# Kernel tuning notes

Measured on AMD Instinct MI355X. Metric: run time of the kernel, lower is better.

## Reference

```python
import jax, jax.numpy as jnp
import numpy as np

B, L, IN = 16, 1024, 128
H, C = 4, 32


def setup_inputs() -> dict:
    key = jax.random.key(0)
    k1, k2, k3, k4, k5, k6 = jax.random.split(key, 6)
    x = jax.random.normal(k1, (B, L, IN), dtype=jnp.float32)
    adj = jax.random.randint(k2, (B, L, L), 0, 2, dtype=jnp.int32)
    # xavier-uniform-ish scales
    s_w = (6.0 / (IN + H * C)) ** 0.5
    W = jax.random.uniform(k3, (H * C, IN), jnp.float32, -s_w, s_w)
    b = jnp.zeros((H * C,), jnp.float32)
    s_a = (6.0 / (1 + C)) ** 0.5
    att_src = jax.random.uniform(k4, (1, H, C), jnp.float32, -s_a, s_a)
    att_dst = jax.random.uniform(k5, (1, H, C), jnp.float32, -s_a, s_a)
    return {"x": x, "adj": adj, "W": W, "b": b, "att_src": att_src, "att_dst": att_dst}


def reference(x, adj, W, b, att_src, att_dst):
    Bx, Lx, _ = x.shape
    Hh, Cc = att_src.shape[1], att_src.shape[2]
    # dropout p=0.0 -> identity
    xp = (x @ W.T + b).reshape(Bx, Lx, Hh, Cc)            # (B,L,H,C)
    a_src = jnp.einsum('blhc,hc->bhl', xp, att_src[0])    # (B,H,L)
    a_dst = jnp.einsum('blhc,hc->bhl', xp, att_dst[0])    # (B,H,L)
    # scores[b,h,i,j] = leaky_relu(a_src[j] + a_dst[i])
    scores = jax.nn.leaky_relu(a_src[:, :, None, :] + a_dst[:, :, :, None], negative_slope=0.2)
    eye = jnp.eye(Lx, dtype=bool)
    mask = jnp.where((adj > 0) | eye, 0.0, -jnp.inf)      # (B,L,L)
    alpha = jax.nn.softmax(scores + mask[:, None, :, :], axis=-1)  # (B,H,L,L)
    out = jnp.einsum('bhij,bjhc->bihc', alpha, xp)        # (B,L,H,C)
    return out.reshape(Bx, Lx, Hh * Cc)
```

## Files before the change

### kernel.cpp

```cpp
#include <hip/hip_runtime.h>
#include <hip/hip_bf16.h>

typedef __bf16 bf16x8 __attribute__((ext_vector_type(8)));
typedef _Float16 f16x8 __attribute__((ext_vector_type(8)));
typedef _Float16 f16x2 __attribute__((ext_vector_type(2)));
typedef float f32x4 __attribute__((ext_vector_type(4)));

#define B_DIM 16
#define L_DIM 1024
#define H_DIM 4
#define HC 128
#define TI 64
#define WPITCH 136

__global__ __launch_bounds__(256) void mask_pack_kernel(
    const int* __restrict__ adj, unsigned* __restrict__ mask_g)
{
  const int t = threadIdx.x;
  const int wv = t >> 6, lane = t & 63;
  const int row0 = blockIdx.x * 8 + wv * 2;
  const int* base = adj + (size_t)row0 * L_DIM;

  int4 av[8];
#pragma unroll
  for (int c = 0; c < 4; ++c) {
    av[c]     = *reinterpret_cast<const int4*>(base + c * 256 + lane * 4);
    av[c + 4] = *reinterpret_cast<const int4*>(base + 1024 + c * 256 + lane * 4);
  }

#pragma unroll
  for (int r = 0; r < 2; ++r) {
    const int row = row0 + r;
    const int i = row & (L_DIM - 1);
#pragma unroll
    for (int c = 0; c < 4; ++c) {
      const int4 u = av[r * 4 + c];
      unsigned b4 = (unsigned)u.x | ((unsigned)u.y << 1) |
                    ((unsigned)u.z << 2) | ((unsigned)u.w << 3);
      unsigned p;
      p = __shfl_xor(b4, 1);
      unsigned b8  = (lane & 1) ? (p | (b4 << 4))   : (b4 | (p << 4));
      p = __shfl_xor(b8, 2);
      unsigned b16 = (lane & 2) ? (p | (b8 << 8))   : (b8 | (p << 8));
      p = __shfl_xor(b16, 4);
      unsigned b32 = (lane & 4) ? (p | (b16 << 16)) : (b16 | (p << 16));
      const int widx = c * 8 + (lane >> 3);
      if ((i >> 5) == widx) b32 |= (1u << (i & 31));
      if ((lane & 7) == 0) mask_g[(size_t)row * 32 + widx] = b32;
    }
  }
}

__global__ __launch_bounds__(128) void proj_kernel(
    const float* __restrict__ x, const float* __restrict__ W,
    const float* __restrict__ bias, const float* __restrict__ att_src,
    const float* __restrict__ att_dst, _Float16* __restrict__ xpT,
    _Float16* __restrict__ E1h, _Float16* __restrict__ E2h,
    float* __restrict__ Rr)
{
  __shared__ __align__(16) __bf16 Wlds[128 * WPITCH];
  __shared__ __align__(16) __bf16 xh[32 * WPITCH];
  __shared__ __align__(16) __bf16 xl[32 * WPITCH];
  const int t = threadIdx.x;
  const int w = t >> 6;
  const int lane = t & 63;
  const int r0 = blockIdx.x * 32;

#pragma unroll
  for (int p = 0; p < 16; ++p) {
    const int idx = p * 1024 + t * 8;
    const int n = idx >> 7, k = idx & 127;
    const f32x4 a = *reinterpret_cast<const f32x4*>(W + idx);
    const f32x4 b = *reinterpret_cast<const f32x4*>(W + idx + 4);
    bf16x8 v;
#pragma unroll
    for (int e = 0; e < 4; ++e) { v[e] = (__bf16)a[e]; v[e + 4] = (__bf16)b[e]; }
    *reinterpret_cast<bf16x8*>(&Wlds[n * WPITCH + k]) = v;
  }
#pragma unroll
  for (int p = 0; p < 4; ++p) {
    const int idx = p * 1024 + t * 8;
    const int r = idx >> 7, k = idx & 127;
    const float* xp_ = x + (size_t)(r0 + r) * 128 + k;
    const f32x4 a = *reinterpret_cast<const f32x4*>(xp_);
    const f32x4 b = *reinterpret_cast<const f32x4*>(xp_ + 4);
    bf16x8 vh, vl;
#pragma unroll
    for (int e = 0; e < 4; ++e) {
      const float fa = a[e], fb = b[e];
      vh[e] = (__bf16)fa;          vh[e + 4] = (__bf16)fb;
      vl[e] = (__bf16)(fa - (float)vh[e]);
      vl[e + 4] = (__bf16)(fb - (float)vh[e + 4]);
    }
    *reinterpret_cast<bf16x8*>(&xh[r * WPITCH + k]) = vh;
    *reinterpret_cast<bf16x8*>(&xl[r * WPITCH + k]) = vl;
  }
  __syncthreads();

  const int rr = lane & 15;
  const int g8 = (lane >> 4) * 8;
  f32x4 acc[8] = {};
#pragma unroll
  for (int kk = 0; kk < 4; ++kk) {
    const int ko = kk * 32 + g8;
    const bf16x8 bh = *reinterpret_cast<const bf16x8*>(&xh[(w * 16 + rr) * WPITCH + ko]);
    const bf16x8 bl = *reinterpret_cast<const bf16x8*>(&xl[(w * 16 + rr) * WPITCH + ko]);
#pragma unroll
    for (int nc = 0; nc < 8; ++nc) {
      const bf16x8 af = *reinterpret_cast<const bf16x8*>(&Wlds[(nc * 16 + rr) * WPITCH + ko]);
      acc[nc] = __builtin_amdgcn_mfma_f32_16x16x32_bf16(af, bh, acc[nc], 0, 0, 0);
      acc[nc] = __builtin_amdgcn_mfma_f32_16x16x32_bf16(af, bl, acc[nc], 0, 0, 0);
    }
  }

  const int q4 = (lane >> 4) * 4;
  const int grow = r0 + w * 16 + rr;
  const int bb = grow >> 10;
  const int lg = grow & 1023;
  float asum[4] = {0.f, 0.f, 0.f, 0.f};
  float adsum[4] = {0.f, 0.f, 0.f, 0.f};
#pragma unroll
  for (int nc = 0; nc < 8; ++nc) {
    const int n0 = nc * 16 + q4;
    const f32x4 bv = *reinterpret_cast<const f32x4*>(bias + n0);
    const f32x4 sv = *reinterpret_cast<const f32x4*>(att_src + n0);
    const f32x4 dv = *reinterpret_cast<const f32x4*>(att_dst + n0);
    const int h = nc >> 1;
#pragma unroll
    for (int reg = 0; reg < 4; ++reg) {
      const float v = acc[nc][reg] + bv[reg];
      const int n = n0 + reg;
      xpT[((size_t)bb * 128 + n) * 1024 + lg] = (_Float16)v;
      asum[h]  = fmaf(v, sv[reg], asum[h]);
      adsum[h] = fmaf(v, dv[reg], adsum[h]);
    }
  }
#pragma unroll
  for (int h = 0; h < 4; ++h) {
    asum[h]  += __shfl_xor(asum[h], 16);
    asum[h]  += __shfl_xor(asum[h], 32);
    adsum[h] += __shfl_xor(adsum[h], 16);
    adsum[h] += __shfl_xor(adsum[h], 32);
  }
  if ((lane >> 4) == 0) {
#pragma unroll
    for (int h = 0; h < 4; ++h) {
      const size_t o = ((size_t)bb * 4 + h) * 1024 + lg;
      E1h[o] = (_Float16)(16.0f * __expf(asum[h]));
      E2h[o] = (_Float16)__expf(0.2f * asum[h]);
      Rr[o]  = 16.0f * __expf(-0.8f * adsum[h]);
    }
  }
}

__global__ __launch_bounds__(512, 4) void gat_attn_kernel(
    const unsigned* __restrict__ mask_g, const _Float16* __restrict__ xpT,
    const _Float16* __restrict__ E1h, const _Float16* __restrict__ E2h,
    const float* __restrict__ Rr, float* __restrict__ out)
{
  __shared__ __align__(16) char smem[53248];
  unsigned* e1u = reinterpret_cast<unsigned*>(smem);
  unsigned* e2u = reinterpret_cast<unsigned*>(smem + 8192);
  unsigned char* msk = reinterpret_cast<unsigned char*>(smem + 16384);
  float* comb = reinterpret_cast<float*>(smem);

  const int wg  = blockIdx.x;
  const int xcd = wg & 7;
  const int idx = wg >> 3;
  const int b   = xcd * 2 + (idx & 1);
  const int i0  = (idx >> 1) * TI;

  const int t = threadIdx.x;
  const int wv = t >> 6;
  const int lane = t & 63;
  const int h  = wv >> 1;
  const int jh = wv & 1;

  {
    const int r = t >> 3, sg = t & 7;
    const uint4 m = *reinterpret_cast<const uint4*>(
        mask_g + ((size_t)b * L_DIM + i0 + r) * 32 + sg * 4);
    *reinterpret_cast<uint4*>(&msk[r * 176 + sg * 16]) = m;
  }
  {
    const int sh = t >> 7;
    const int off = (t & 127) * 8;
    const _Float16* p1 = E1h + ((size_t)(b * H_DIM + sh)) * L_DIM + off;
    const _Float16* p2 = E2h + ((size_t)(b * H_DIM + sh)) * L_DIM + off;
    *reinterpret_cast<uint4*>(&e1u[sh * 512 + (off >> 1)]) = *reinterpret_cast<const uint4*>(p1);
    *reinterpret_cast<uint4*>(&e2u[sh * 512 + (off >> 1)]) = *reinterpret_cast<const uint4*>(p2);
  }
  __syncthreads();

  const int ln15 = lane & 15;
  const int kh = lane >> 4;
  const int jb = kh * 8;
  const int base = jh * 512;
  const float* RrB = Rr + ((size_t)(b * H_DIM + h)) * L_DIM + i0 + ln15;
  f16x2 R2g[4];
#pragma unroll
  for (int g = 0; g < 4; ++g) {
    const _Float16 rh = (_Float16)RrB[g * 16];
    R2g[g][0] = rh; R2g[g][1] = rh;
  }
  const _Float16* xb0 = xpT + ((size_t)(b * 128 + h * 32 + ln15)) * 1024 + base;
  const _Float16* xb1 = xb0 + 16 * 1024;

  f32x4 acc0[4] = {}, acc1[4] = {}, accS[4] = {};
  f16x8 ones16;
#pragma unroll
  for (int e = 0; e < 8; ++e) ones16[e] = (_Float16)1.0f;

  uint4 pf0[2], pf1[2];
#pragma unroll
  for (int s = 0; s < 2; ++s) {
    pf0[s] = *reinterpret_cast<const uint4*>(xb0 + s * 32 + jb);
    pf1[s] = *reinterpret_cast<const uint4*>(xb1 + s * 32 + jb);
  }
  uint4 u1c = *reinterpret_cast<const uint4*>(&e1u[h * 512 + ((base + jb) >> 1)]);
  uint4 u2c = *reinterpret_cast<const uint4*>(&e2u[h * 512 + ((base + jb) >> 1)]);

#pragma unroll 4
  for (int kr = 0; kr < 512; kr += 32) {
    const int k0 = base + kr;
    const int wb = jh * 64 + ((kr >> 5) << 2);
    unsigned mb[4];
#pragma unroll
    for (int g = 0; g < 4; ++g) {
      const unsigned w32 = *reinterpret_cast<const unsigned*>(
          &msk[(g * 16 + ln15) * 176 + wb]);
      mb[g] = (w32 >> (kh * 8)) & 0xffu;
    }

    const int kn = (((k0 + 32) & 1023) + jb) >> 1;
    const uint4 u1n = *reinterpret_cast<const uint4*>(&e1u[h * 512 + kn]);
    const uint4 u2n = *reinterpret_cast<const uint4*>(&e2u[h * 512 + kn]);

    const int sl = (kr >> 5) & 1;
    const uint4 bb0 = pf0[sl];
    const uint4 bb1 = pf1[sl];
    pf0[sl] = *reinterpret_cast<const uint4*>(xb0 + kr + 64 + jb);
    pf1[sl] = *reinterpret_cast<const uint4*>(xb1 + kr + 64 + jb);

    const unsigned uu1[4] = {u1c.x, u1c.y, u1c.z, u1c.w};
    const unsigned uu2[4] = {u2c.x, u2c.y, u2c.z, u2c.w};
    unsigned rg[4][4];
#pragma unroll
    for (int q = 0; q < 4; ++q) {
      f16x2 a, ee;
      __builtin_memcpy(&a,  &uu1[q], 4);
      __builtin_memcpy(&ee, &uu2[q], 4);
#pragma unroll
      for (int g = 0; g < 4; ++g) {
        const f16x2 pr = ee * R2g[g];
        const f16x2 mx = __builtin_elementwise_max(a, pr);
        unsigned mu;
        __builtin_memcpy(&mu, &mx, 4);
        const unsigned mlo = (mb[g] & (1u << (2 * q)))     ? 0xFFFFu : 0u;
        const unsigned mhi = (mb[g] & (1u << (2 * q + 1))) ? 0xFFFF0000u : 0u;
        rg[g][q] = mu & (mlo | mhi);
      }
    }
    f16x8 b0h, b1h;
    __builtin_memcpy(&b0h, &bb0, 16);
    __builtin_memcpy(&b1h, &bb1, 16);
#pragma unroll
    for (int g = 0; g < 4; ++g) {
      const uint4 afu = {rg[g][0], rg[g][1], rg[g][2], rg[g][3]};
      f16x8 af;
      __builtin_memcpy(&af, &afu, 16);
      acc0[g] = __builtin_amdgcn_mfma_f32_16x16x32_f16(af, b0h, acc0[g], 0, 0, 0);
      acc1[g] = __builtin_amdgcn_mfma_f32_16x16x32_f16(af, b1h, acc1[g], 0, 0, 0);
      accS[g] = __builtin_amdgcn_mfma_f32_16x16x32_f16(af, ones16, accS[g], 0, 0, 0);
    }
    u1c = u1n; u2c = u2n;
  }

  __syncthreads();
  if (jh == 1) {
#pragma unroll
    for (int g = 0; g < 4; ++g) {
      float* cp = &comb[((h * 4 + g) * 64 + lane) * 13];
#pragma unroll
      for (int e = 0; e < 4; ++e) {
        cp[e]     = acc0[g][e];
        cp[4 + e] = acc1[g][e];
        cp[8 + e] = accS[g][e];
      }
    }
  }
  __syncthreads();
  if (jh == 0) {
#pragma unroll
    for (int g = 0; g < 4; ++g) {
      const float* cp = &comb[((h * 4 + g) * 64 + lane) * 13];
#pragma unroll
      for (int reg = 0; reg < 4; ++reg) {
        const float s = accS[g][reg] + cp[8 + reg];
        const float rs = 1.0f / s;
        float* op = out + ((size_t)(b * L_DIM + i0 + g * 16 + kh * 4 + reg)) * HC + h * 32;
        op[ln15]      = (acc0[g][reg] + cp[reg])     * rs;
        op[16 + ln15] = (acc1[g][reg] + cp[4 + reg]) * rs;
      }
    }
  }
}

extern "C" void kernel_launch(void* const* d_in, const int* in_sizes, int n_in,
                              void* d_out, int out_size, void* d_ws, size_t ws_size,
                              hipStream_t stream) {
  (void)in_sizes; (void)n_in; (void)out_size; (void)ws_size;
  const float* x        = (const float*)d_in[0];
  const int*   adj      = (const int*)d_in[1];
  const float* W        = (const float*)d_in[2];
  const float* bias     = (const float*)d_in[3];
  const float* att_src  = (const float*)d_in[4];
  const float* att_dst  = (const float*)d_in[5];
  float* out = (float*)d_out;

  char* ws = (char*)d_ws;
  _Float16* xpT    = (_Float16*)ws;
  _Float16* E1h    = (_Float16*)(ws + (size_t)4 * 1024 * 1024);
  _Float16* E2h    = (_Float16*)(ws + (size_t)4 * 1024 * 1024 + 131072);
  float*    Rr     = (float*)(ws + (size_t)4 * 1024 * 1024 + 262144);
  unsigned* mask_g = (unsigned*)(ws + (size_t)4 * 1024 * 1024 + 524288);

  hipLaunchKernelGGL(mask_pack_kernel, dim3(B_DIM * L_DIM / 8), dim3(256), 0, stream,
                     adj, mask_g);
  hipLaunchKernelGGL(proj_kernel, dim3(B_DIM * L_DIM / 32), dim3(128), 0, stream,
                     x, W, bias, att_src, att_dst, xpT, E1h, E2h, Rr);
  hipLaunchKernelGGL(gat_attn_kernel, dim3(B_DIM * L_DIM / TI), dim3(512), 0, stream,
                     mask_g, xpT, E1h, E2h, Rr, out);
}
```

Measured before the change: 41.33 us.

## Merge mask-pack and projection kernels; split attention key range across four waves

```diff
diff --git a/kernel.cpp b/kernel.cpp
--- a/kernel.cpp
+++ b/kernel.cpp
@@ -12,63 +12,60 @@
 #define HC 128
 #define TI 64
 #define WPITCH 136
-
-__global__ __launch_bounds__(256) void mask_pack_kernel(
-    const int* __restrict__ adj, unsigned* __restrict__ mask_g)
+#define PROJ_BLOCKS 256
+
+__global__ __launch_bounds__(256) void prep_kernel(
+    const float* __restrict__ x, const float* __restrict__ W,
+    const float* __restrict__ bias, const float* __restrict__ att_src,
+    const float* __restrict__ att_dst, const int* __restrict__ adj,
+    _Float16* __restrict__ xpT, _Float16* __restrict__ E1h,
+    _Float16* __restrict__ E2h, float* __restrict__ Rr,
+    unsigned* __restrict__ mask_g)
 {
+  __shared__ __align__(16) __bf16 Wlds[128 * WPITCH];
+  __shared__ __align__(16) __bf16 xh[64 * WPITCH];
+  __shared__ __align__(16) __bf16 xl[64 * WPITCH];
+  const int bid = blockIdx.x;
   const int t = threadIdx.x;
   const int wv = t >> 6, lane = t & 63;
-  const int row0 = blockIdx.x * 8 + wv * 2;
-  const int* base = adj + (size_t)row0 * L_DIM;
-
-  int4 av[8];
-#pragma unroll
-  for (int c = 0; c < 4; ++c) {
-    av[c]     = *reinterpret_cast<const int4*>(base + c * 256 + lane * 4);
-    av[c + 4] = *reinterpret_cast<const int4*>(base + 1024 + c * 256 + lane * 4);
-  }
-
-#pragma unroll
-  for (int r = 0; r < 2; ++r) {
-    const int row = row0 + r;
-    const int i = row & (L_DIM - 1);
+
+  if (bid >= PROJ_BLOCKS) {
+    const int row0 = (bid - PROJ_BLOCKS) * 8 + wv * 2;
+    const int* base = adj + (size_t)row0 * L_DIM;
+    int4 av[8];
 #pragma unroll
     for (int c = 0; c < 4; ++c) {
-      const int4 u = av[r * 4 + c];
-      unsigned b4 = (unsigned)u.x | ((unsigned)u.y << 1) |
-                    ((unsigned)u.z << 2) | ((unsigned)u.w << 3);
-      unsigned p;
-      p = __shfl_xor(b4, 1);
-      unsigned b8  = (lane & 1) ? (p | (b4 << 4))   : (b4 | (p << 4));
-      p = __shfl_xor(b8, 2);
-      unsigned b16 = (lane & 2) ? (p | (b8 << 8))   : (b8 | (p << 8));
-      p = __shfl_xor(b16, 4);
-      unsigned b32 = (lane & 4) ? (p | (b16 << 16)) : (b16 | (p << 16));
-      const int widx = c * 8 + (lane >> 3);
-      if ((i >> 5) == widx) b32 |= (1u << (i & 31));
-      if ((lane & 7) == 0) mask_g[(size_t)row * 32 + widx] = b32;
-    }
-  }
-}
-
-__global__ __launch_bounds__(128) void proj_kernel(
-    const float* __restrict__ x, const float* __restrict__ W,
-    const float* __restrict__ bias, const float* __restrict__ att_src,
-    const float* __restrict__ att_dst, _Float16* __restrict__ xpT,
-    _Float16* __restrict__ E1h, _Float16* __restrict__ E2h,
-    float* __restrict__ Rr)
-{
-  __shared__ __align__(16) __bf16 Wlds[128 * WPITCH];
-  __shared__ __align__(16) __bf16 xh[32 * WPITCH];
-  __shared__ __align__(16) __bf16 xl[32 * WPITCH];
-  const int t = threadIdx.x;
-  const int w = t >> 6;
-  const int lane = t & 63;
-  const int r0 = blockIdx.x * 32;
-
-#pragma unroll
-  for (int p = 0; p < 16; ++p) {
-    const int idx = p * 1024 + t * 8;
+      av[c]     = *reinterpret_cast<const int4*>(base + c * 256 + lane * 4);
+      av[c + 4] = *reinterpret_cast<const int4*>(base + 1024 + c * 256 + lane * 4);
+    }
+#pragma unroll
+    for (int r = 0; r < 2; ++r) {
+      const int row = row0 + r;
+      const int i = row & (L_DIM - 1);
+#pragma unroll
+      for (int c = 0; c < 4; ++c) {
+        const int4 u = av[r * 4 + c];
+        unsigned b4 = (unsigned)u.x | ((unsigned)u.y << 1) |
+                      ((unsigned)u.z << 2) | ((unsigned)u.w << 3);
+        unsigned p;
+        p = __shfl_xor(b4, 1);
+        unsigned b8  = (lane & 1) ? (p | (b4 << 4))   : (b4 | (p << 4));
+        p = __shfl_xor(b8, 2);
+        unsigned b16 = (lane & 2) ? (p | (b8 << 8))   : (b8 | (p << 8));
+        p = __shfl_xor(b16, 4);
+        unsigned b32 = (lane & 4) ? (p | (b16 << 16)) : (b16 | (p << 16));
+        const int widx = c * 8 + (lane >> 3);
+        if ((i >> 5) == widx) b32 |= (1u << (i & 31));
+        if ((lane & 7) == 0) mask_g[(size_t)row * 32 + widx] = b32;
+      }
+    }
+    return;
+  }
+
+  const int r0 = bid * 64;
+#pragma unroll
+  for (int p = 0; p < 8; ++p) {
+    const int idx = p * 2048 + t * 8;
     const int n = idx >> 7, k = idx & 127;
     const f32x4 a = *reinterpret_cast<const f32x4*>(W + idx);
     const f32x4 b = *reinterpret_cast<const f32x4*>(W + idx + 4);
@@ -79,7 +76,7 @@
   }
 #pragma unroll
   for (int p = 0; p < 4; ++p) {
-    const int idx = p * 1024 + t * 8;
+    const int idx = p * 2048 + t * 8;
     const int r = idx >> 7, k = idx & 127;
     const float* xp_ = x + (size_t)(r0 + r) * 128 + k;
     const f32x4 a = *reinterpret_cast<const f32x4*>(xp_);
@@ -103,8 +100,8 @@
 #pragma unroll
   for (int kk = 0; kk < 4; ++kk) {
     const int ko = kk * 32 + g8;
-    const bf16x8 bh = *reinterpret_cast<const bf16x8*>(&xh[(w * 16 + rr) * WPITCH + ko]);
-    const bf16x8 bl = *reinterpret_cast<const bf16x8*>(&xl[(w * 16 + rr) * WPITCH + ko]);
+    const bf16x8 bh = *reinterpret_cast<const bf16x8*>(&xh[(wv * 16 + rr) * WPITCH + ko]);
+    const bf16x8 bl = *reinterpret_cast<const bf16x8*>(&xl[(wv * 16 + rr) * WPITCH + ko]);
 #pragma unroll
     for (int nc = 0; nc < 8; ++nc) {
       const bf16x8 af = *reinterpret_cast<const bf16x8*>(&Wlds[(nc * 16 + rr) * WPITCH + ko]);
@@ -114,7 +111,7 @@
   }
 
   const int q4 = (lane >> 4) * 4;
-  const int grow = r0 + w * 16 + rr;
+  const int grow = r0 + wv * 16 + rr;
   const int bb = grow >> 10;
   const int lg = grow & 1023;
   float asum[4] = {0.f, 0.f, 0.f, 0.f};
@@ -153,7 +150,7 @@
   }
 }
 
-__global__ __launch_bounds__(512, 4) void gat_attn_kernel(
+__global__ __launch_bounds__(1024, 4) void gat_attn_kernel(
     const unsigned* __restrict__ mask_g, const _Float16* __restrict__ xpT,
     const _Float16* __restrict__ E1h, const _Float16* __restrict__ E2h,
     const float* __restrict__ Rr, float* __restrict__ out)
@@ -173,29 +170,29 @@
   const int t = threadIdx.x;
   const int wv = t >> 6;
   const int lane = t & 63;
-  const int h  = wv >> 1;
-  const int jh = wv & 1;
+  const int h  = wv >> 2;
+  const int jq = wv & 3;
 
   {
-    const int r = t >> 3, sg = t & 7;
-    const uint4 m = *reinterpret_cast<const uint4*>(
-        mask_g + ((size_t)b * L_DIM + i0 + r) * 32 + sg * 4);
-    *reinterpret_cast<uint4*>(&msk[r * 176 + sg * 16]) = m;
+    const int r = t >> 4, sg = t & 15;
+    const uint2 m = *reinterpret_cast<const uint2*>(
+        mask_g + ((size_t)b * L_DIM + i0 + r) * 32 + sg * 2);
+    *reinterpret_cast<uint2*>(&msk[r * 176 + sg * 8]) = m;
   }
   {
-    const int sh = t >> 7;
-    const int off = (t & 127) * 8;
+    const int sh = t >> 8;
+    const int off = (t & 255) * 4;
     const _Float16* p1 = E1h + ((size_t)(b * H_DIM + sh)) * L_DIM + off;
     const _Float16* p2 = E2h + ((size_t)(b * H_DIM + sh)) * L_DIM + off;
-    *reinterpret_cast<uint4*>(&e1u[sh * 512 + (off >> 1)]) = *reinterpret_cast<const uint4*>(p1);
-    *reinterpret_cast<uint4*>(&e2u[sh * 512 + (off >> 1)]) = *reinterpret_cast<const uint4*>(p2);
+    *reinterpret_cast<uint2*>(&e1u[sh * 512 + (off >> 1)]) = *reinterpret_cast<const uint2*>(p1);
+    *reinterpret_cast<uint2*>(&e2u[sh * 512 + (off >> 1)]) = *reinterpret_cast<const uint2*>(p2);
   }
   __syncthreads();
 
   const int ln15 = lane & 15;
   const int kh = lane >> 4;
   const int jb = kh * 8;
-  const int base = jh * 512;
+  const int base = jq * 256;
   const float* RrB = Rr + ((size_t)(b * H_DIM + h)) * L_DIM + i0 + ln15;
   f16x2 R2g[4];
 #pragma unroll
@@ -221,9 +218,9 @@
   uint4 u2c = *reinterpret_cast<const uint4*>(&e2u[h * 512 + ((base + jb) >> 1)]);
 
 #pragma unroll 4
-  for (int kr = 0; kr < 512; kr += 32) {
+  for (int kr = 0; kr < 256; kr += 32) {
     const int k0 = base + kr;
-    const int wb = jh * 64 + ((kr >> 5) << 2);
+    const int wb = jq * 32 + ((kr >> 5) << 2);
     unsigned mb[4];
 #pragma unroll
     for (int g = 0; g < 4; ++g) {
@@ -277,30 +274,29 @@
   }
 
   __syncthreads();
-  if (jh == 1) {
-#pragma unroll
-    for (int g = 0; g < 4; ++g) {
-      float* cp = &comb[((h * 4 + g) * 64 + lane) * 13];
-#pragma unroll
-      for (int e = 0; e < 4; ++e) {
-        cp[e]     = acc0[g][e];
-        cp[4 + e] = acc1[g][e];
-        cp[8 + e] = accS[g][e];
-      }
-    }
-  }
-  __syncthreads();
-  if (jh == 0) {
+  for (int i = t; i < 4 * 4 * 64 * 13; i += 1024) comb[i] = 0.0f;
+  __syncthreads();
+#pragma unroll
+  for (int g = 0; g < 4; ++g) {
+    float* cp = &comb[((h * 4 + g) * 64 + lane) * 13];
+#pragma unroll
+    for (int e = 0; e < 4; ++e) {
+      atomicAdd(&cp[e],     acc0[g][e]);
+      atomicAdd(&cp[4 + e], acc1[g][e]);
+      atomicAdd(&cp[8 + e], accS[g][e]);
+    }
+  }
+  __syncthreads();
+  if (jq == 0) {
 #pragma unroll
     for (int g = 0; g < 4; ++g) {
       const float* cp = &comb[((h * 4 + g) * 64 + lane) * 13];
 #pragma unroll
       for (int reg = 0; reg < 4; ++reg) {
-        const float s = accS[g][reg] + cp[8 + reg];
-        const float rs = 1.0f / s;
+        const float rs = 1.0f / cp[8 + reg];
         float* op = out + ((size_t)(b * L_DIM + i0 + g * 16 + kh * 4 + reg)) * HC + h * 32;
-        op[ln15]      = (acc0[g][reg] + cp[reg])     * rs;
-        op[16 + ln15] = (acc1[g][reg] + cp[4 + reg]) * rs;
+        op[ln15]      = cp[reg]     * rs;
+        op[16 + ln15] = cp[4 + reg] * rs;
       }
     }
   }
@@ -325,10 +321,8 @@
   float*    Rr     = (float*)(ws + (size_t)4 * 1024 * 1024 + 262144);
   unsigned* mask_g = (unsigned*)(ws + (size_t)4 * 1024 * 1024 + 524288);
 
-  hipLaunchKernelGGL(mask_pack_kernel, dim3(B_DIM * L_DIM / 8), dim3(256), 0, stream,
-                     adj, mask_g);
-  hipLaunchKernelGGL(proj_kernel, dim3(B_DIM * L_DIM / 32), dim3(128), 0, stream,
-                     x, W, bias, att_src, att_dst, xpT, E1h, E2h, Rr);
-  hipLaunchKernelGGL(gat_attn_kernel, dim3(B_DIM * L_DIM / TI), dim3(512), 0, stream,
+  hipLaunchKernelGGL(prep_kernel, dim3(PROJ_BLOCKS + B_DIM * L_DIM / 8), dim3(256), 0, stream,
+                     x, W, bias, att_src, att_dst, adj, xpT, E1h, E2h, Rr, mask_g);
+  hipLaunchKernelGGL(gat_attn_kernel, dim3(B_DIM * L_DIM / TI), dim3(1024), 0, stream,
                      mask_g, xpT, E1h, E2h, Rr, out);
 }
```

Result: slower. 97.94 us (+137.0%).

## Split attention heads across two workgroups and quarter the key range per wave

Applied to the files above, without the earlier changes.

```diff
diff --git a/kernel.cpp b/kernel.cpp
--- a/kernel.cpp
+++ b/kernel.cpp
@@ -158,23 +158,26 @@
     const _Float16* __restrict__ E1h, const _Float16* __restrict__ E2h,
     const float* __restrict__ Rr, float* __restrict__ out)
 {
-  __shared__ __align__(16) char smem[53248];
+  __shared__ __align__(16) char smem[79872];
   unsigned* e1u = reinterpret_cast<unsigned*>(smem);
-  unsigned* e2u = reinterpret_cast<unsigned*>(smem + 8192);
-  unsigned char* msk = reinterpret_cast<unsigned char*>(smem + 16384);
+  unsigned* e2u = reinterpret_cast<unsigned*>(smem + 4096);
+  unsigned char* msk = reinterpret_cast<unsigned char*>(smem + 8192);
   float* comb = reinterpret_cast<float*>(smem);
 
   const int wg  = blockIdx.x;
   const int xcd = wg & 7;
   const int idx = wg >> 3;
   const int b   = xcd * 2 + (idx & 1);
-  const int i0  = (idx >> 1) * TI;
+  const int it  = idx >> 1;
+  const int hp  = it & 1;
+  const int i0  = (it >> 1) * TI;
 
   const int t = threadIdx.x;
   const int wv = t >> 6;
   const int lane = t & 63;
-  const int h  = wv >> 1;
-  const int jh = wv & 1;
+  const int hh = wv >> 2;
+  const int h  = hp * 2 + hh;
+  const int jq = wv & 3;
 
   {
     const int r = t >> 3, sg = t & 7;
@@ -183,19 +186,19 @@
     *reinterpret_cast<uint4*>(&msk[r * 176 + sg * 16]) = m;
   }
   {
-    const int sh = t >> 7;
-    const int off = (t & 127) * 8;
-    const _Float16* p1 = E1h + ((size_t)(b * H_DIM + sh)) * L_DIM + off;
-    const _Float16* p2 = E2h + ((size_t)(b * H_DIM + sh)) * L_DIM + off;
-    *reinterpret_cast<uint4*>(&e1u[sh * 512 + (off >> 1)]) = *reinterpret_cast<const uint4*>(p1);
-    *reinterpret_cast<uint4*>(&e2u[sh * 512 + (off >> 1)]) = *reinterpret_cast<const uint4*>(p2);
+    const int sh = t >> 8;
+    const int off = (t & 255) * 4;
+    const _Float16* p1 = E1h + ((size_t)(b * H_DIM + hp * 2 + sh)) * L_DIM + off;
+    const _Float16* p2 = E2h + ((size_t)(b * H_DIM + hp * 2 + sh)) * L_DIM + off;
+    *reinterpret_cast<uint2*>(&e1u[sh * 512 + (off >> 1)]) = *reinterpret_cast<const uint2*>(p1);
+    *reinterpret_cast<uint2*>(&e2u[sh * 512 + (off >> 1)]) = *reinterpret_cast<const uint2*>(p2);
   }
   __syncthreads();
 
   const int ln15 = lane & 15;
   const int kh = lane >> 4;
   const int jb = kh * 8;
-  const int base = jh * 512;
+  const int base = jq * 256;
   const float* RrB = Rr + ((size_t)(b * H_DIM + h)) * L_DIM + i0 + ln15;
   f16x2 R2g[4];
 #pragma unroll
@@ -217,13 +220,13 @@
     pf0[s] = *reinterpret_cast<const uint4*>(xb0 + s * 32 + jb);
     pf1[s] = *reinterpret_cast<const uint4*>(xb1 + s * 32 + jb);
   }
-  uint4 u1c = *reinterpret_cast<const uint4*>(&e1u[h * 512 + ((base + jb) >> 1)]);
-  uint4 u2c = *reinterpret_cast<const uint4*>(&e2u[h * 512 + ((base + jb) >> 1)]);
+  uint4 u1c = *reinterpret_cast<const uint4*>(&e1u[hh * 512 + ((base + jb) >> 1)]);
+  uint4 u2c = *reinterpret_cast<const uint4*>(&e2u[hh * 512 + ((base + jb) >> 1)]);
 
 #pragma unroll 4
-  for (int kr = 0; kr < 512; kr += 32) {
+  for (int kr = 0; kr < 256; kr += 32) {
     const int k0 = base + kr;
-    const int wb = jh * 64 + ((kr >> 5) << 2);
+    const int wb = jq * 32 + ((kr >> 5) << 2);
     unsigned mb[4];
 #pragma unroll
     for (int g = 0; g < 4; ++g) {
@@ -233,8 +236,8 @@
     }
 
     const int kn = (((k0 + 32) & 1023) + jb) >> 1;
-    const uint4 u1n = *reinterpret_cast<const uint4*>(&e1u[h * 512 + kn]);
-    const uint4 u2n = *reinterpret_cast<const uint4*>(&e2u[h * 512 + kn]);
+    const uint4 u1n = *reinterpret_cast<const uint4*>(&e1u[hh * 512 + kn]);
+    const uint4 u2n = *reinterpret_cast<const uint4*>(&e2u[hh * 512 + kn]);
 
     const int sl = (kr >> 5) & 1;
     const uint4 bb0 = pf0[sl];
@@ -277,10 +280,10 @@
   }
 
   __syncthreads();
-  if (jh == 1) {
+  if (jq != 0) {
 #pragma unroll
     for (int g = 0; g < 4; ++g) {
-      float* cp = &comb[((h * 4 + g) * 64 + lane) * 13];
+      float* cp = &comb[(((hh * 3 + (jq - 1)) * 4 + g) * 64 + lane) * 13];
 #pragma unroll
       for (int e = 0; e < 4; ++e) {
         cp[e]     = acc0[g][e];
@@ -290,17 +293,26 @@
     }
   }
   __syncthreads();
-  if (jh == 0) {
+  if (jq == 0) {
 #pragma unroll
     for (int g = 0; g < 4; ++g) {
-      const float* cp = &comb[((h * 4 + g) * 64 + lane) * 13];
+      f32x4 s0 = acc0[g], s1 = acc1[g], sS = accS[g];
+#pragma unroll
+      for (int p = 0; p < 3; ++p) {
+        const float* cp = &comb[(((hh * 3 + p) * 4 + g) * 64 + lane) * 13];
+#pragma unroll
+        for (int e = 0; e < 4; ++e) {
+          s0[e] += cp[e];
+          s1[e] += cp[4 + e];
+          sS[e] += cp[8 + e];
+        }
+      }
 #pragma unroll
       for (int reg = 0; reg < 4; ++reg) {
-        const float s = accS[g][reg] + cp[8 + reg];
-        const float rs = 1.0f / s;
+        const float rs = 1.0f / sS[reg];
         float* op = out + ((size_t)(b * L_DIM + i0 + g * 16 + kh * 4 + reg)) * HC + h * 32;
-        op[ln15]      = (acc0[g][reg] + cp[reg])     * rs;
-        op[16 + ln15] = (acc1[g][reg] + cp[4 + reg]) * rs;
+        op[ln15]      = s0[reg] * rs;
+        op[16 + ln15] = s1[reg] * rs;
       }
     }
   }
@@ -329,6 +341,6 @@
                      adj, mask_g);
   hipLaunchKernelGGL(proj_kernel, dim3(B_DIM * L_DIM / 32), dim3(128), 0, stream,
                      x, W, bias, att_src, att_dst, xpT, E1h, E2h, Rr);
-  hipLaunchKernelGGL(gat_attn_kernel, dim3(B_DIM * L_DIM / TI), dim3(512), 0, stream,
+  hipLaunchKernelGGL(gat_attn_kernel, dim3(2 * B_DIM * L_DIM / TI), dim3(512), 0, stream,
                      mask_g, xpT, E1h, E2h, Rr, out);
 }
```

Measured after the change: 49.32 us. 19.3% more time.

## Fuse adjacency bit-packing into attention kernel with chunked double-buffered mask

Applied to the files above, without the earlier changes.

```diff
diff --git a/kernel.cpp b/kernel.cpp
--- a/kernel.cpp
+++ b/kernel.cpp
@@ -12,44 +12,6 @@
 #define HC 128
 #define TI 64
 #define WPITCH 136
-
-__global__ __launch_bounds__(256) void mask_pack_kernel(
-    const int* __restrict__ adj, unsigned* __restrict__ mask_g)
-{
-  const int t = threadIdx.x;
-  const int wv = t >> 6, lane = t & 63;
-  const int row0 = blockIdx.x * 8 + wv * 2;
-  const int* base = adj + (size_t)row0 * L_DIM;
-
-  int4 av[8];
-#pragma unroll
-  for (int c = 0; c < 4; ++c) {
-    av[c]     = *reinterpret_cast<const int4*>(base + c * 256 + lane * 4);
-    av[c + 4] = *reinterpret_cast<const int4*>(base + 1024 + c * 256 + lane * 4);
-  }
-
-#pragma unroll
-  for (int r = 0; r < 2; ++r) {
-    const int row = row0 + r;
-    const int i = row & (L_DIM - 1);
-#pragma unroll
-    for (int c = 0; c < 4; ++c) {
-      const int4 u = av[r * 4 + c];
-      unsigned b4 = (unsigned)u.x | ((unsigned)u.y << 1) |
-                    ((unsigned)u.z << 2) | ((unsigned)u.w << 3);
-      unsigned p;
-      p = __shfl_xor(b4, 1);
-      unsigned b8  = (lane & 1) ? (p | (b4 << 4))   : (b4 | (p << 4));
-      p = __shfl_xor(b8, 2);
-      unsigned b16 = (lane & 2) ? (p | (b8 << 8))   : (b8 | (p << 8));
-      p = __shfl_xor(b16, 4);
-      unsigned b32 = (lane & 4) ? (p | (b16 << 16)) : (b16 | (p << 16));
-      const int widx = c * 8 + (lane >> 3);
-      if ((i >> 5) == widx) b32 |= (1u << (i & 31));
-      if ((lane & 7) == 0) mask_g[(size_t)row * 32 + widx] = b32;
-    }
-  }
-}
 
 __global__ __launch_bounds__(128) void proj_kernel(
     const float* __restrict__ x, const float* __restrict__ W,
@@ -153,16 +115,14 @@
   }
 }
 
-__global__ __launch_bounds__(512, 4) void gat_attn_kernel(
-    const unsigned* __restrict__ mask_g, const _Float16* __restrict__ xpT,
+__global__ __launch_bounds__(512, 2) void gat_attn_kernel(
+    const int* __restrict__ adj, const _Float16* __restrict__ xpT,
     const _Float16* __restrict__ E1h, const _Float16* __restrict__ E2h,
     const float* __restrict__ Rr, float* __restrict__ out)
 {
-  __shared__ __align__(16) char smem[53248];
-  unsigned* e1u = reinterpret_cast<unsigned*>(smem);
-  unsigned* e2u = reinterpret_cast<unsigned*>(smem + 8192);
-  unsigned char* msk = reinterpret_cast<unsigned char*>(smem + 16384);
-  float* comb = reinterpret_cast<float*>(smem);
+  __shared__ __align__(16) unsigned e1u[H_DIM][512];
+  __shared__ __align__(16) unsigned e2u[H_DIM][512];
+  __shared__ __align__(16) unsigned short msk[2][64][8];
 
   const int wg  = blockIdx.x;
   const int xcd = wg & 7;
@@ -174,136 +134,161 @@
   const int wv = t >> 6;
   const int lane = t & 63;
   const int h  = wv >> 1;
-  const int jh = wv & 1;
-
-  {
-    const int r = t >> 3, sg = t & 7;
-    const uint4 m = *reinterpret_cast<const uint4*>(
-        mask_g + ((size_t)b * L_DIM + i0 + r) * 32 + sg * 4);
-    *reinterpret_cast<uint4*>(&msk[r * 176 + sg * 16]) = m;
-  }
+  const int rh = wv & 1;
+  const int ln15 = lane & 15;
+  const int kh = lane >> 4;
+  const int jb = kh * 8;
+
+  const int pr = t >> 3;
+  const int ps = t & 7;
+  const int gi = i0 + pr;
+  const int* arow = adj + ((size_t)b * L_DIM + gi) * L_DIM + ps * 16;
+
+  int4 av[4];
+#define LOAD_CHUNK(c)                                                    \
+  {                                                                      \
+    _Pragma("unroll")                                                    \
+    for (int q = 0; q < 4; ++q)                                          \
+      av[q] = *reinterpret_cast<const int4*>(arow + (c) * 128 + q * 4);  \
+  }
+#define PACK_CHUNK(c, buf)                                               \
+  {                                                                      \
+    unsigned bits = 0;                                                   \
+    _Pragma("unroll")                                                    \
+    for (int q = 0; q < 4; ++q) {                                        \
+      const int4 u = av[q];                                              \
+      const unsigned b4 = (unsigned)u.x | ((unsigned)u.y << 1) |         \
+                          ((unsigned)u.z << 2) | ((unsigned)u.w << 3);   \
+      bits |= b4 << (q * 4);                                             \
+    }                                                                    \
+    const int d = gi - ((c) * 128 + ps * 16);                            \
+    if ((unsigned)d < 16u) bits |= (1u << d);                            \
+    msk[buf][pr][ps] = (unsigned short)bits;                             \
+  }
+
+  LOAD_CHUNK(0);
   {
     const int sh = t >> 7;
     const int off = (t & 127) * 8;
     const _Float16* p1 = E1h + ((size_t)(b * H_DIM + sh)) * L_DIM + off;
     const _Float16* p2 = E2h + ((size_t)(b * H_DIM + sh)) * L_DIM + off;
-    *reinterpret_cast<uint4*>(&e1u[sh * 512 + (off >> 1)]) = *reinterpret_cast<const uint4*>(p1);
-    *reinterpret_cast<uint4*>(&e2u[sh * 512 + (off >> 1)]) = *reinterpret_cast<const uint4*>(p2);
-  }
-  __syncthreads();
-
-  const int ln15 = lane & 15;
-  const int kh = lane >> 4;
-  const int jb = kh * 8;
-  const int base = jh * 512;
-  const float* RrB = Rr + ((size_t)(b * H_DIM + h)) * L_DIM + i0 + ln15;
-  f16x2 R2g[4];
-#pragma unroll
-  for (int g = 0; g < 4; ++g) {
-    const _Float16 rh = (_Float16)RrB[g * 16];
-    R2g[g][0] = rh; R2g[g][1] = rh;
-  }
-  const _Float16* xb0 = xpT + ((size_t)(b * 128 + h * 32 + ln15)) * 1024 + base;
+    *reinterpret_cast<uint4*>(&e1u[sh][off >> 1]) = *reinterpret_cast<const uint4*>(p1);
+    *reinterpret_cast<uint4*>(&e2u[sh][off >> 1]) = *reinterpret_cast<const uint4*>(p2);
+  }
+  PACK_CHUNK(0, 0);
+  LOAD_CHUNK(1);
+
+  const float* RrB = Rr + ((size_t)(b * H_DIM + h)) * L_DIM + i0 + rh * 32 + ln15;
+  f16x2 R2g[2];
+#pragma unroll
+  for (int g = 0; g < 2; ++g) {
+    const _Float16 rv = (_Float16)RrB[g * 16];
+    R2g[g][0] = rv; R2g[g][1] = rv;
+  }
+  const _Float16* xb0 = xpT + ((size_t)(b * 128 + h * 32 + ln15)) * 1024;
   const _Float16* xb1 = xb0 + 16 * 1024;
 
-  f32x4 acc0[4] = {}, acc1[4] = {}, accS[4] = {};
-  f16x8 ones16;
-#pragma unroll
-  for (int e = 0; e < 8; ++e) ones16[e] = (_Float16)1.0f;
-
-  uint4 pf0[2], pf1[2];
-#pragma unroll
-  for (int s = 0; s < 2; ++s) {
+  uint4 pf0[4], pf1[4];
+#pragma unroll
+  for (int s = 0; s < 4; ++s) {
     pf0[s] = *reinterpret_cast<const uint4*>(xb0 + s * 32 + jb);
     pf1[s] = *reinterpret_cast<const uint4*>(xb1 + s * 32 + jb);
   }
-  uint4 u1c = *reinterpret_cast<const uint4*>(&e1u[h * 512 + ((base + jb) >> 1)]);
-  uint4 u2c = *reinterpret_cast<const uint4*>(&e2u[h * 512 + ((base + jb) >> 1)]);
-
-#pragma unroll 4
-  for (int kr = 0; kr < 512; kr += 32) {
-    const int k0 = base + kr;
-    const int wb = jh * 64 + ((kr >> 5) << 2);
-    unsigned mb[4];
-#pragma unroll
-    for (int g = 0; g < 4; ++g) {
-      const unsigned w32 = *reinterpret_cast<const unsigned*>(
-          &msk[(g * 16 + ln15) * 176 + wb]);
-      mb[g] = (w32 >> (kh * 8)) & 0xffu;
-    }
-
-    const int kn = (((k0 + 32) & 1023) + jb) >> 1;
-    const uint4 u1n = *reinterpret_cast<const uint4*>(&e1u[h * 512 + kn]);
-    const uint4 u2n = *reinterpret_cast<const uint4*>(&e2u[h * 512 + kn]);
-
-    const int sl = (kr >> 5) & 1;
-    const uint4 bb0 = pf0[sl];
-    const uint4 bb1 = pf1[sl];
-    pf0[sl] = *reinterpret_cast<const uint4*>(xb0 + kr + 64 + jb);
-    pf1[sl] = *reinterpret_cast<const uint4*>(xb1 + kr + 64 + jb);
-
-    const unsigned uu1[4] = {u1c.x, u1c.y, u1c.z, u1c.w};
-    const unsigned uu2[4] = {u2c.x, u2c.y, u2c.z, u2c.w};
-    unsigned rg[4][4];
-#pragma unroll
-    for (int q = 0; q < 4; ++q) {
-      f16x2 a, ee;
-      __builtin_memcpy(&a,  &uu1[q], 4);
-      __builtin_memcpy(&ee, &uu2[q], 4);
-#pragma unroll
-      for (int g = 0; g < 4; ++g) {
-        const f16x2 pr = ee * R2g[g];
-        const f16x2 mx = __builtin_elementwise_max(a, pr);
-        unsigned mu;
-        __builtin_memcpy(&mu, &mx, 4);
-        const unsigned mlo = (mb[g] & (1u << (2 * q)))     ? 0xFFFFu : 0u;
-        const unsigned mhi = (mb[g] & (1u << (2 * q + 1))) ? 0xFFFF0000u : 0u;
-        rg[g][q] = mu & (mlo | mhi);
+  __syncthreads();
+
+  uint4 u1r[2], u2r[2];
+#pragma unroll
+  for (int s = 0; s < 2; ++s) {
+    const int ke = (s * 32 + jb) >> 1;
+    u1r[s] = *reinterpret_cast<const uint4*>(&e1u[h][ke]);
+    u2r[s] = *reinterpret_cast<const uint4*>(&e2u[h][ke]);
+  }
+
+  f32x4 acc0[2] = {}, acc1[2] = {}, accS[2] = {};
+  f16x8 ones16;
+#pragma unroll
+  for (int e = 0; e < 8; ++e) ones16[e] = (_Float16)1.0f;
+
+  int cbuf = 0;
+  for (int c = 0; c < 8; ++c) {
+    uint4 mwcA = *reinterpret_cast<const uint4*>(&msk[cbuf][rh * 32 + ln15][0]);
+    uint4 mwcB = *reinterpret_cast<const uint4*>(&msk[cbuf][rh * 32 + 16 + ln15][0]);
+    if (c < 7) PACK_CHUNK(c + 1, cbuf ^ 1);
+    if (c < 6) LOAD_CHUNK(c + 2);
+
+#pragma unroll
+    for (int it = 0; it < 4; ++it) {
+      const int kr = c * 128 + it * 32;
+      const unsigned wA = (it == 0) ? mwcA.x : (it == 1) ? mwcA.y
+                        : (it == 2) ? mwcA.z : mwcA.w;
+      const unsigned wB = (it == 0) ? mwcB.x : (it == 1) ? mwcB.y
+                        : (it == 2) ? mwcB.z : mwcB.w;
+      unsigned mb[2];
+      mb[0] = (wA >> (kh * 8)) & 0xffu;
+      mb[1] = (wB >> (kh * 8)) & 0xffu;
+
+      const uint4 u1c = u1r[it & 1];
+      const uint4 u2c = u2r[it & 1];
+      const int kn = (((kr + 64) & 1023) + jb) >> 1;
+      u1r[it & 1] = *reinterpret_cast<const uint4*>(&e1u[h][kn]);
+      u2r[it & 1] = *reinterpret_cast<const uint4*>(&e2u[h][kn]);
+
+      const uint4 bb0 = pf0[it];
+      const uint4 bb1 = pf1[it];
+      pf0[it] = *reinterpret_cast<const uint4*>(xb0 + kr + 128 + jb);
+      pf1[it] = *reinterpret_cast<const uint4*>(xb1 + kr + 128 + jb);
+
+      const unsigned uu1[4] = {u1c.x, u1c.y, u1c.z, u1c.w};
+      const unsigned uu2[4] = {u2c.x, u2c.y, u2c.z, u2c.w};
+      unsigned rg[2][4];
+#pragma unroll
+      for (int q = 0; q < 4; ++q) {
+        f16x2 a, ee;
+        __builtin_memcpy(&a,  &uu1[q], 4);
+        __builtin_memcpy(&ee, &uu2[q], 4);
+#pragma unroll
+        for (int g = 0; g < 2; ++g) {
+          const f16x2 pr2 = ee * R2g[g];
+          const f16x2 mx = __builtin_elementwise_max(a, pr2);
+          unsigned mu;
+          __builtin_memcpy(&mu, &mx, 4);
+          const unsigned mlo = (mb[g] & (1u << (2 * q)))     ? 0xFFFFu : 0u;
+          const unsigned mhi = (mb[g] & (1u << (2 * q + 1))) ? 0xFFFF0000u : 0u;
+          rg[g][q] = mu & (mlo | mhi);
+        }
       }
-    }
-    f16x8 b0h, b1h;
-    __builtin_memcpy(&b0h, &bb0, 16);
-    __builtin_memcpy(&b1h, &bb1, 16);
-#pragma unroll
-    for (int g = 0; g < 4; ++g) {
-      const uint4 afu = {rg[g][0], rg[g][1], rg[g][2], rg[g][3]};
-      f16x8 af;
-      __builtin_memcpy(&af, &afu, 16);
-      acc0[g] = __builtin_amdgcn_mfma_f32_16x16x32_f16(af, b0h, acc0[g], 0, 0, 0);
-      acc1[g] = __builtin_amdgcn_mfma_f32_16x16x32_f16(af, b1h, acc1[g], 0, 0, 0);
-      accS[g] = __builtin_amdgcn_mfma_f32_16x16x32_f16(af, ones16, accS[g], 0, 0, 0);
-    }
-    u1c = u1n; u2c = u2n;
-  }
-
-  __syncthreads();
-  if (jh == 1) {
-#pragma unroll
-    for (int g = 0; g < 4; ++g) {
-      float* cp = &comb[((h * 4 + g) * 64 + lane) * 13];
-#pragma unroll
-      for (int e = 0; e < 4; ++e) {
-        cp[e]     = acc0[g][e];
-        cp[4 + e] = acc1[g][e];
-        cp[8 + e] = accS[g][e];
+      f16x8 b0h, b1h;
+      __builtin_memcpy(&b0h, &bb0, 16);
+      __builtin_memcpy(&b1h, &bb1, 16);
+      __builtin_amdgcn_s_setprio(1);
+#pragma unroll
+      for (int g = 0; g < 2; ++g) {
+        const uint4 afu = {rg[g][0], rg[g][1], rg[g][2], rg[g][3]};
+        f16x8 af;
+        __builtin_memcpy(&af, &afu, 16);
+        acc0[g] = __builtin_amdgcn_mfma_f32_16x16x32_f16(af, b0h, acc0[g], 0, 0, 0);
+        acc1[g] = __builtin_amdgcn_mfma_f32_16x16x32_f16(af, b1h, acc1[g], 0, 0, 0);
+        accS[g] = __builtin_amdgcn_mfma_f32_16x16x32_f16(af, ones16, accS[g], 0, 0, 0);
       }
-    }
-  }
-  __syncthreads();
-  if (jh == 0) {
-#pragma unroll
-    for (int g = 0; g < 4; ++g) {
-      const float* cp = &comb[((h * 4 + g) * 64 + lane) * 13];
-#pragma unroll
-      for (int reg = 0; reg < 4; ++reg) {
-        const float s = accS[g][reg] + cp[8 + reg];
-        const float rs = 1.0f / s;
-        float* op = out + ((size_t)(b * L_DIM + i0 + g * 16 + kh * 4 + reg)) * HC + h * 32;
-        op[ln15]      = (acc0[g][reg] + cp[reg])     * rs;
-        op[16 + ln15] = (acc1[g][reg] + cp[4 + reg]) * rs;
-      }
-    }
-  }
+      __builtin_amdgcn_s_setprio(0);
+    }
+    __syncthreads();
+    cbuf ^= 1;
+  }
+
+#pragma unroll
+  for (int g = 0; g < 2; ++g) {
+#pragma unroll
+    for (int reg = 0; reg < 4; ++reg) {
+      const float rs = 1.0f / accS[g][reg];
+      const int row = i0 + rh * 32 + g * 16 + kh * 4 + reg;
+      float* op = out + ((size_t)(b * L_DIM + row)) * HC + h * 32;
+      op[ln15]      = acc0[g][reg] * rs;
+      op[16 + ln15] = acc1[g][reg] * rs;
+    }
+  }
+#undef LOAD_CHUNK
+#undef PACK_CHUNK
 }
 
 extern "C" void kernel_launch(void* const* d_in, const int* in_sizes, int n_in,
@@ -319,16 +304,13 @@
   float* out = (float*)d_out;
 
   char* ws = (char*)d_ws;
-  _Float16* xpT    = (_Float16*)ws;
-  _Float16* E1h    = (_Float16*)(ws + (size_t)4 * 1024 * 1024);
-  _Float16* E2h    = (_Float16*)(ws + (size_t)4 * 1024 * 1024 + 131072);
-  float*    Rr     = (float*)(ws + (size_t)4 * 1024 * 1024 + 262144);
-  unsigned* mask_g = (unsigned*)(ws + (size_t)4 * 1024 * 1024 + 524288);
-
-  hipLaunchKernelGGL(mask_pack_kernel, dim3(B_DIM * L_DIM / 8), dim3(256), 0, stream,
-                     adj, mask_g);
+  _Float16* xpT = (_Float16*)ws;
+  _Float16* E1h = (_Float16*)(ws + (size_t)4 * 1024 * 1024);
+  _Float16* E2h = (_Float16*)(ws + (size_t)4 * 1024 * 1024 + 131072);
+  float*    Rr  = (float*)(ws + (size_t)4 * 1024 * 1024 + 262144);
+
   hipLaunchKernelGGL(proj_kernel, dim3(B_DIM * L_DIM / 32), dim3(128), 0, stream,
                      x, W, bias, att_src, att_dst, xpT, E1h, E2h, Rr);
   hipLaunchKernelGGL(gat_attn_kernel, dim3(B_DIM * L_DIM / TI), dim3(512), 0, stream,
-                     mask_g, xpT, E1h, E2h, Rr, out);
+                     adj, xpT, E1h, E2h, Rr, out);
 }
```

Result: faster. 34.14 us, median of 2 (-17.4%).
